# Optimization experiments

Hardware: AMD Instinct MI355X
Metric: run time of the kernel (lower is better)

Reference implementation:

```python
import jax, jax.numpy as jnp
import numpy as np

N_SRC = 50000   # e.g. users
N_DST = 50000   # e.g. items
N = N_SRC + N_DST
E = 1_600_000   # edges (avg degree ~16)
D = 64          # in_size == out_size


def _xavier(key, shape):
    # xavier_uniform for Linear(weight shape [out, in])
    fan_out, fan_in = shape
    limit = jnp.sqrt(6.0 / (fan_in + fan_out)).astype(jnp.float32)
    return jax.random.uniform(key, shape, jnp.float32, -limit, limit)


def setup_inputs() -> dict:
    key = jax.random.key(0)
    ks = jax.random.split(key, 8)
    return {
        "src_embedding": jax.random.normal(ks[0], (N_SRC, D), jnp.float32),
        "dst_embedding": jax.random.normal(ks[1], (N_DST, D), jnp.float32),
        "norm": jax.random.uniform(ks[2], (E, 1), jnp.float32),
        "W1": _xavier(ks[3], (D, D)),
        "b1": jnp.zeros((D,), jnp.float32),
        "W2": _xavier(ks[4], (D, D)),
        "b2": jnp.zeros((D,), jnp.float32),
        "edges_src": jax.random.randint(ks[5], (E,), 0, N, dtype=jnp.int32),
        "edges_dst": jax.random.randint(ks[6], (E,), 0, N, dtype=jnp.int32),
    }


def reference(src_embedding, dst_embedding, norm, W1, b1, W2, b2,
              edges_src, edges_dst):
    # concat user/item node tables: [N, D]
    x = jnp.concatenate([src_embedding, dst_embedding], axis=0)
    xs = x[edges_src]                      # [E, D] gather (edge source nodes)
    xd = x[edges_dst]                      # [E, D] gather (edge dest nodes)
    # msgs = W1(x_src) + W2(x_src * x_dst), per edge
    msgs = (jnp.einsum('ed,od->eo', xs, W1) + b1
            + jnp.einsum('ed,od->eo', xs * xd, W2) + b2)   # [E, D]
    msgs = norm * msgs                     # per-edge scalar normalization
    # copy_e + sum: scatter-sum messages onto destination nodes
    h = jax.ops.segment_sum(msgs, edges_dst, num_segments=N)  # [N, D]
    # LeakyReLU(0.2); dropout is identity in eval / p=0
    return jnp.where(h > 0, h, 0.2 * h)
```

## Files before the change

### kernel.cpp

```cpp
#include <hip/hip_runtime.h>
#include <hip/hip_bf16.h>


#define CHUNK 4096
#define NBMAX 1024
#define BCAP  2304

typedef __attribute__((ext_vector_type(8))) short short8v;
typedef __attribute__((ext_vector_type(4))) float f32x4;
union U4S8 { uint4 u; short8v s; };

__device__ __forceinline__ unsigned int f2bf(float f) {
    unsigned int u = __float_as_uint(f);
    u += 0x7fffu + ((u >> 16) & 1u);
    return u >> 16;
}
__device__ __forceinline__ unsigned int pkbf(float lo, float hi) {
    return (f2bf(hi) << 16) | f2bf(lo);
}

__global__ __launch_bounds__(256) void prep_init_kernel(
    const float* __restrict__ srcEmb, const float* __restrict__ dstEmb,
    unsigned int* __restrict__ xbf, int* __restrict__ gcur,
    int Ntot, int n_src, int NB)
{
    int i = blockIdx.x * 256 + threadIdx.x;
    if (i < NB) gcur[i] = i * BCAP;
    if (i >= Ntot * 32) return;
    int n = i >> 5, w = i & 31;
    const float* row = (n < n_src) ? srcEmb + (size_t)n * 64
                                   : dstEmb + (size_t)(n - n_src) * 64;
    xbf[i] = (f2bf(row[w + 32]) << 16) | f2bf(row[w]);
}

__global__ __launch_bounds__(1024) void part_scatter_kernel(
    const int* __restrict__ es, const int* __restrict__ ed,
    const float* __restrict__ norm, int* __restrict__ gcur,
    uint2* __restrict__ epk, int E, int NB)
{
    __shared__ int   bcnt[NBMAX];
    __shared__ int   lstart[NBMAX];
    __shared__ int   gbase[NBMAX];
    __shared__ int   sc[NBMAX];
    __shared__ uint2 sorted[CHUNK];

    int t  = threadIdx.x;
    int e0 = blockIdx.x * CHUNK;

    bcnt[t] = 0;
    __syncthreads();

    int dreg[4];
    #pragma unroll
    for (int k = 0; k < 4; ++k) {
        int e = e0 + t + k * 1024;
        dreg[k] = (e < E) ? ed[e] : -1;
        if (dreg[k] >= 0) atomicAdd(&bcnt[dreg[k] >> 7], 1);
    }
    __syncthreads();

    int c = (t < NB) ? bcnt[t] : 0;
    sc[t] = c;
    __syncthreads();
    for (int off = 1; off < NBMAX; off <<= 1) {
        int x = 0;
        if (t >= off) x = sc[t - off];
        __syncthreads();
        if (t >= off) sc[t] += x;
        __syncthreads();
    }
    int ex = sc[t] - c;
    lstart[t] = ex;
    bcnt[t]   = ex;
    if (c > 0) gbase[t] = atomicAdd(&gcur[t], c);
    __syncthreads();

    #pragma unroll
    for (int k = 0; k < 4; ++k) {
        int e = e0 + t + k * 1024;
        if (dreg[k] >= 0) {
            unsigned int q = (unsigned int)(norm[e] * 32767.f + 0.5f);
            if (q > 32767u) q = 32767u;
            int lp = atomicAdd(&bcnt[dreg[k] >> 7], 1);
            uint2 r; r.x = (unsigned int)es[e];
            r.y = ((unsigned int)dreg[k] << 15) | q;
            sorted[lp] = r;
        }
    }
    __syncthreads();

    int total = E - e0; if (total > CHUNK) total = CHUNK;
    for (int i = t; i < total; i += 1024) {
        uint2 r = sorted[i];
        int b = (int)(r.y >> 22);
        int gpos = gbase[b] + (i - lstart[b]);
        if (gpos < (b + 1) * BCAP)
            epk[gpos] = r;
    }
}

__global__ __launch_bounds__(512) void bucket_sort_kernel(
    const int* __restrict__ gcur, const uint2* __restrict__ epk,
    uint2* __restrict__ epk2, int* __restrict__ offsets2)
{
    __shared__ int bh[128];
    __shared__ int sc[128];

    int b = blockIdx.x, t = threadIdx.x;
    int base  = b * BCAP;
    int total = gcur[b] - base;
    if (total > BCAP) total = BCAP;

    if (t < 128) bh[t] = 0;
    __syncthreads();
    for (int i = t; i < total; i += 512)
        atomicAdd(&bh[(epk[base + i].y >> 15) & 127], 1);
    __syncthreads();

    int v = 0;
    if (t < 128) { v = bh[t]; sc[t] = v; }
    __syncthreads();
    for (int off = 1; off < 128; off <<= 1) {
        int x = 0;
        if (t < 128 && t >= off) x = sc[t - off];
        __syncthreads();
        if (t < 128 && t >= off) sc[t] += x;
        __syncthreads();
    }
    if (t < 128) {
        int ex = sc[t] - v;
        offsets2[b * 129 + t] = ex;
        if (t == 127) offsets2[b * 129 + 128] = sc[127];
        bh[t] = ex;
    }
    __syncthreads();

    for (int i = t; i < total; i += 512) {
        uint2 r = epk[base + i];
        int pos = atomicAdd(&bh[(r.y >> 15) & 127], 1);
        epk2[base + pos] = r;
    }
}

__global__ __launch_bounds__(256) void accumulate_kernel(
    const unsigned int* __restrict__ xbf,
    const int* __restrict__ offsets2, const uint2* __restrict__ epk2,
    unsigned int* __restrict__ Acat, float* __restrict__ cnt, int Ntot)
{
    int idx  = blockIdx.x * 256 + threadIdx.x;
    int n    = idx >> 6;
    int lane = idx & 63;
    if (n >= Ntot) return;
    int sl  = lane & 7;
    int g   = lane >> 3;
    int b   = n >> 7;
    int loc = n & 127;

    int s0 = b * BCAP + offsets2[b * 129 + loc];
    int s1 = b * BCAP + offsets2[b * 129 + loc + 1];

    float ax0 = 0.f, ax1 = 0.f, ax2 = 0.f, ax3 = 0.f;
    float ay0 = 0.f, ay1 = 0.f, ay2 = 0.f, ay3 = 0.f;
    float c = 0.f;

    for (int base = s0; base < s1; base += 64) {
        int m = s1 - base; if (m > 64) m = 64;
        unsigned int px = 0u, py = 0u;
        if (lane < m) { uint2 pk = epk2[base + lane]; px = pk.x; py = pk.y; }
        for (int k = 0; k < m; k += 16) {
            unsigned int sx0 = __shfl(px, k + g);
            unsigned int sy0 = __shfl(py, k + g);
            unsigned int sx1 = __shfl(px, k + 8 + g);
            unsigned int sy1 = __shfl(py, k + 8 + g);
            uint4 u0 = *(const uint4*)(xbf + (size_t)sx0 * 32 + 4 * sl);
            uint4 u1 = *(const uint4*)(xbf + (size_t)sx1 * 32 + 4 * sl);
            float w0 = (float)(sy0 & 0x7fffu) * (1.f / 32767.f);
            float w1 = (float)(sy1 & 0x7fffu) * (1.f / 32767.f);
            ax0 = fmaf(w0, __uint_as_float(u0.x << 16), ax0);
            ax1 = fmaf(w0, __uint_as_float(u0.y << 16), ax1);
            ax2 = fmaf(w0, __uint_as_float(u0.z << 16), ax2);
            ax3 = fmaf(w0, __uint_as_float(u0.w << 16), ax3);
            ay0 = fmaf(w0, __uint_as_float(u0.x & 0xffff0000u), ay0);
            ay1 = fmaf(w0, __uint_as_float(u0.y & 0xffff0000u), ay1);
            ay2 = fmaf(w0, __uint_as_float(u0.z & 0xffff0000u), ay2);
            ay3 = fmaf(w0, __uint_as_float(u0.w & 0xffff0000u), ay3);
            c += w0;
            ax0 = fmaf(w1, __uint_as_float(u1.x << 16), ax0);
            ax1 = fmaf(w1, __uint_as_float(u1.y << 16), ax1);
            ax2 = fmaf(w1, __uint_as_float(u1.z << 16), ax2);
            ax3 = fmaf(w1, __uint_as_float(u1.w << 16), ax3);
            ay0 = fmaf(w1, __uint_as_float(u1.x & 0xffff0000u), ay0);
            ay1 = fmaf(w1, __uint_as_float(u1.y & 0xffff0000u), ay1);
            ay2 = fmaf(w1, __uint_as_float(u1.z & 0xffff0000u), ay2);
            ay3 = fmaf(w1, __uint_as_float(u1.w & 0xffff0000u), ay3);
            c += w1;
        }
    }

    #pragma unroll
    for (int off = 8; off < 64; off <<= 1) {
        ax0 += __shfl_xor(ax0, off); ax1 += __shfl_xor(ax1, off);
        ax2 += __shfl_xor(ax2, off); ax3 += __shfl_xor(ax3, off);
        ay0 += __shfl_xor(ay0, off); ay1 += __shfl_xor(ay1, off);
        ay2 += __shfl_xor(ay2, off); ay3 += __shfl_xor(ay3, off);
        c   += __shfl_xor(c,   off);
    }

    if (g == 0) {
        uint4 xv = *(const uint4*)(xbf + (size_t)n * 32 + 4 * sl);
        float xl0 = __uint_as_float(xv.x << 16);
        float xl1 = __uint_as_float(xv.y << 16);
        float xl2 = __uint_as_float(xv.z << 16);
        float xl3 = __uint_as_float(xv.w << 16);
        float xh0 = __uint_as_float(xv.x & 0xffff0000u);
        float xh1 = __uint_as_float(xv.y & 0xffff0000u);
        float xh2 = __uint_as_float(xv.z & 0xffff0000u);
        float xh3 = __uint_as_float(xv.w & 0xffff0000u);

        uint4 w0;
        w0.x = pkbf(ax0, ax1);
        w0.y = pkbf(ax2, ax3);
        w0.z = pkbf(ay0, ay1);
        w0.w = pkbf(ay2, ay3);
        uint4 w1;
        w1.x = pkbf(ax0 * xl0, ax1 * xl1);
        w1.y = pkbf(ax2 * xl2, ax3 * xl3);
        w1.z = pkbf(ay0 * xh0, ay1 * xh1);
        w1.w = pkbf(ay2 * xh2, ay3 * xh3);
        *(uint4*)(Acat + (size_t)n * 64 + 4 * sl)      = w0;
        *(uint4*)(Acat + (size_t)n * 64 + 32 + 4 * sl) = w1;
        if (sl == 0) cnt[n] = c;
    }
}

__global__ __launch_bounds__(256) void node_gemm_kernel(
    const unsigned int* __restrict__ Acat, const float* __restrict__ cnt,
    const float* __restrict__ W1, const float* __restrict__ b1,
    const float* __restrict__ W2, const float* __restrict__ b2,
    float* __restrict__ out, int Ntot)
{
    __shared__ unsigned int wlds[64 * 68];

    int t     = threadIdx.x;
    int lane  = t & 63;
    int wv    = t >> 6;
    int base  = blockIdx.x * 64;
    int row16 = lane & 15;
    int q     = lane >> 4;

    int arow = base + wv * 16 + row16;
    if (arow >= Ntot) arow = Ntot - 1;
    const uint4* ap = (const uint4*)(Acat + (size_t)arow * 64);
    uint4 af[4];
    #pragma unroll
    for (int s = 0; s < 4; ++s) af[s] = ap[s * 4 + q];

    for (int i = t; i < 64 * 64; i += 256) {
        int o = i >> 6, j = i & 63;
        int jj = j & 31, sl = jj >> 2, tt = jj & 3;
        int d0 = 4 * sl + ((tt & 1) << 1) + ((tt & 2) ? 32 : 0);
        const float* wsrc = (j < 32) ? W1 : W2;
        wlds[o * 68 + j] = pkbf(wsrc[o * 64 + d0], wsrc[o * 64 + d0 + 1]);
    }

    float cload[4];
    #pragma unroll
    for (int r = 0; r < 4; ++r) {
        int grow = base + wv * 16 + q * 4 + r;
        cload[r] = cnt[grow < Ntot ? grow : (Ntot - 1)];
    }
    f32x4 acc[4];
    #pragma unroll
    for (int j = 0; j < 4; ++j) {
        int col = j * 16 + row16;
        float bs = b1[col] + b2[col];
        #pragma unroll
        for (int r = 0; r < 4; ++r) acc[j][r] = cload[r] * bs;
    }
    __syncthreads();

    #pragma unroll
    for (int s = 0; s < 4; ++s) {
        U4S8 a; a.u = af[s];
        #pragma unroll
        for (int j = 0; j < 4; ++j) {
            int o = j * 16 + row16;
            U4S8 bb; bb.u = *(const uint4*)(wlds + o * 68 + s * 16 + q * 4);
            acc[j] = __builtin_amdgcn_mfma_f32_16x16x32_bf16(
                a.s, bb.s, acc[j], 0, 0, 0);
        }
    }

    #pragma unroll
    for (int r = 0; r < 4; ++r) {
        int grow = base + wv * 16 + q * 4 + r;
        if (grow < Ntot) {
            #pragma unroll
            for (int j = 0; j < 4; ++j) {
                float a = acc[j][r];
                out[(size_t)grow * 64 + j * 16 + row16] = (a > 0.f) ? a : 0.2f * a;
            }
        }
    }
}

extern "C" void kernel_launch(void* const* d_in, const int* in_sizes, int n_in,
                              void* d_out, int out_size, void* d_ws, size_t ws_size,
                              hipStream_t stream) {
    const float* srcEmb = (const float*)d_in[0];
    const float* dstEmb = (const float*)d_in[1];
    const float* norm   = (const float*)d_in[2];
    const float* W1     = (const float*)d_in[3];
    const float* b1     = (const float*)d_in[4];
    const float* W2     = (const float*)d_in[5];
    const float* b2     = (const float*)d_in[6];
    const int*   es     = (const int*)d_in[7];
    const int*   ed     = (const int*)d_in[8];

    const int n_src = in_sizes[0] / 64;
    const int n_dst = in_sizes[1] / 64;
    const int Ntot  = n_src + n_dst;
    const int E     = in_sizes[7];
    const int NB    = (Ntot + 127) >> 7;

    float* cnt      = (float*)d_ws;
    int*   gcur     = (int*)(cnt + Ntot);
    int*   offsets2 = gcur + NB;
    size_t off4     = (size_t)Ntot + NB + (size_t)NB * 129;
    off4 = (off4 + 3) & ~(size_t)3;
    uint2* epk      = (uint2*)((float*)d_ws + off4);
    uint2* epk2     = epk + (size_t)NB * BCAP;
    unsigned int* xbf = (unsigned int*)(epk2 + (size_t)NB * BCAP);
    unsigned int* Acat = (unsigned int*)d_out;

    prep_init_kernel<<<(Ntot * 32 + 255) / 256, 256, 0, stream>>>(
        srcEmb, dstEmb, xbf, gcur, Ntot, n_src, NB);

    part_scatter_kernel<<<(E + CHUNK - 1) / CHUNK, 1024, 0, stream>>>(
        es, ed, norm, gcur, epk, E, NB);

    bucket_sort_kernel<<<NB, 512, 0, stream>>>(gcur, epk, epk2, offsets2);

    accumulate_kernel<<<(Ntot + 3) / 4, 256, 0, stream>>>(
        xbf, offsets2, epk2, Acat, cnt, Ntot);

    node_gemm_kernel<<<(Ntot + 63) / 64, 256, 0, stream>>>(
        Acat, cnt, W1, b1, W2, b2, (float*)d_out, Ntot);
}
```

Baseline: 198.5 us.

## Map one node per 8 lanes in accumulate kernel instead of per wavefront

The accumulate kernel now assigns each destination node to 8 threads instead of a full 64-lane wavefront. Each 8-lane group walks that node's edges sequentially, two at a time, so the cross-group shuffle reduction and the idle lanes in low-degree nodes go away. Launch size shrinks to match. The cost is that lanes in a wavefront now handle different nodes with different degrees, which adds divergence. Each edge record is also loaded redundantly by the 8 lanes of a group.

Result: slower. 206.9 us (+4.2%).

```diff
diff --git a/kernel.cpp b/kernel.cpp
--- a/kernel.cpp
+++ b/kernel.cpp
@@ -147,12 +147,10 @@
     const int* __restrict__ offsets2, const uint2* __restrict__ epk2,
     unsigned int* __restrict__ Acat, float* __restrict__ cnt, int Ntot)
 {
-    int idx  = blockIdx.x * 256 + threadIdx.x;
-    int n    = idx >> 6;
-    int lane = idx & 63;
+    int idx = blockIdx.x * 256 + threadIdx.x;
+    int n   = idx >> 3;
     if (n >= Ntot) return;
-    int sl  = lane & 7;
-    int g   = lane >> 3;
+    int sl  = threadIdx.x & 7;
     int b   = n >> 7;
     int loc = n & 127;
 
@@ -163,74 +161,56 @@
     float ay0 = 0.f, ay1 = 0.f, ay2 = 0.f, ay3 = 0.f;
     float c = 0.f;
 
-    for (int base = s0; base < s1; base += 64) {
-        int m = s1 - base; if (m > 64) m = 64;
-        unsigned int px = 0u, py = 0u;
-        if (lane < m) { uint2 pk = epk2[base + lane]; px = pk.x; py = pk.y; }
-        for (int k = 0; k < m; k += 16) {
-            unsigned int sx0 = __shfl(px, k + g);
-            unsigned int sy0 = __shfl(py, k + g);
-            unsigned int sx1 = __shfl(px, k + 8 + g);
-            unsigned int sy1 = __shfl(py, k + 8 + g);
-            uint4 u0 = *(const uint4*)(xbf + (size_t)sx0 * 32 + 4 * sl);
-            uint4 u1 = *(const uint4*)(xbf + (size_t)sx1 * 32 + 4 * sl);
-            float w0 = (float)(sy0 & 0x7fffu) * (1.f / 32767.f);
-            float w1 = (float)(sy1 & 0x7fffu) * (1.f / 32767.f);
-            ax0 = fmaf(w0, __uint_as_float(u0.x << 16), ax0);
-            ax1 = fmaf(w0, __uint_as_float(u0.y << 16), ax1);
-            ax2 = fmaf(w0, __uint_as_float(u0.z << 16), ax2);
-            ax3 = fmaf(w0, __uint_as_float(u0.w << 16), ax3);
-            ay0 = fmaf(w0, __uint_as_float(u0.x & 0xffff0000u), ay0);
-            ay1 = fmaf(w0, __uint_as_float(u0.y & 0xffff0000u), ay1);
-            ay2 = fmaf(w0, __uint_as_float(u0.z & 0xffff0000u), ay2);
-            ay3 = fmaf(w0, __uint_as_float(u0.w & 0xffff0000u), ay3);
-            c += w0;
-            ax0 = fmaf(w1, __uint_as_float(u1.x << 16), ax0);
-            ax1 = fmaf(w1, __uint_as_float(u1.y << 16), ax1);
-            ax2 = fmaf(w1, __uint_as_float(u1.z << 16), ax2);
-            ax3 = fmaf(w1, __uint_as_float(u1.w << 16), ax3);
-            ay0 = fmaf(w1, __uint_as_float(u1.x & 0xffff0000u), ay0);
-            ay1 = fmaf(w1, __uint_as_float(u1.y & 0xffff0000u), ay1);
-            ay2 = fmaf(w1, __uint_as_float(u1.z & 0xffff0000u), ay2);
-            ay3 = fmaf(w1, __uint_as_float(u1.w & 0xffff0000u), ay3);
-            c += w1;
-        }
-    }
-
-    #pragma unroll
-    for (int off = 8; off < 64; off <<= 1) {
-        ax0 += __shfl_xor(ax0, off); ax1 += __shfl_xor(ax1, off);
-        ax2 += __shfl_xor(ax2, off); ax3 += __shfl_xor(ax3, off);
-        ay0 += __shfl_xor(ay0, off); ay1 += __shfl_xor(ay1, off);
-        ay2 += __shfl_xor(ay2, off); ay3 += __shfl_xor(ay3, off);
-        c   += __shfl_xor(c,   off);
-    }
-
-    if (g == 0) {
-        uint4 xv = *(const uint4*)(xbf + (size_t)n * 32 + 4 * sl);
-        float xl0 = __uint_as_float(xv.x << 16);
-        float xl1 = __uint_as_float(xv.y << 16);
-        float xl2 = __uint_as_float(xv.z << 16);
-        float xl3 = __uint_as_float(xv.w << 16);
-        float xh0 = __uint_as_float(xv.x & 0xffff0000u);
-        float xh1 = __uint_as_float(xv.y & 0xffff0000u);
-        float xh2 = __uint_as_float(xv.z & 0xffff0000u);
-        float xh3 = __uint_as_float(xv.w & 0xffff0000u);
-
-        uint4 w0;
-        w0.x = pkbf(ax0, ax1);
-        w0.y = pkbf(ax2, ax3);
-        w0.z = pkbf(ay0, ay1);
-        w0.w = pkbf(ay2, ay3);
-        uint4 w1;
-        w1.x = pkbf(ax0 * xl0, ax1 * xl1);
-        w1.y = pkbf(ax2 * xl2, ax3 * xl3);
-        w1.z = pkbf(ay0 * xh0, ay1 * xh1);
-        w1.w = pkbf(ay2 * xh2, ay3 * xh3);
-        *(uint4*)(Acat + (size_t)n * 64 + 4 * sl)      = w0;
-        *(uint4*)(Acat + (size_t)n * 64 + 32 + 4 * sl) = w1;
-        if (sl == 0) cnt[n] = c;
-    }
+    for (int r = s0; r < s1; r += 2) {
+        uint2 p0 = epk2[r];
+        int ok1  = (r + 1 < s1);
+        uint2 p1 = epk2[ok1 ? r + 1 : r];
+        uint4 u0 = *(const uint4*)(xbf + (size_t)p0.x * 32 + 4 * sl);
+        uint4 u1 = *(const uint4*)(xbf + (size_t)p1.x * 32 + 4 * sl);
+        float w0 = (float)(p0.y & 0x7fffu) * (1.f / 32767.f);
+        float w1 = ok1 ? (float)(p1.y & 0x7fffu) * (1.f / 32767.f) : 0.f;
+        ax0 = fmaf(w0, __uint_as_float(u0.x << 16), ax0);
+        ax1 = fmaf(w0, __uint_as_float(u0.y << 16), ax1);
+        ax2 = fmaf(w0, __uint_as_float(u0.z << 16), ax2);
+        ax3 = fmaf(w0, __uint_as_float(u0.w << 16), ax3);
+        ay0 = fmaf(w0, __uint_as_float(u0.x & 0xffff0000u), ay0);
+        ay1 = fmaf(w0, __uint_as_float(u0.y & 0xffff0000u), ay1);
+        ay2 = fmaf(w0, __uint_as_float(u0.z & 0xffff0000u), ay2);
+        ay3 = fmaf(w0, __uint_as_float(u0.w & 0xffff0000u), ay3);
+        ax0 = fmaf(w1, __uint_as_float(u1.x << 16), ax0);
+        ax1 = fmaf(w1, __uint_as_float(u1.y << 16), ax1);
+        ax2 = fmaf(w1, __uint_as_float(u1.z << 16), ax2);
+        ax3 = fmaf(w1, __uint_as_float(u1.w << 16), ax3);
+        ay0 = fmaf(w1, __uint_as_float(u1.x & 0xffff0000u), ay0);
+        ay1 = fmaf(w1, __uint_as_float(u1.y & 0xffff0000u), ay1);
+        ay2 = fmaf(w1, __uint_as_float(u1.z & 0xffff0000u), ay2);
+        ay3 = fmaf(w1, __uint_as_float(u1.w & 0xffff0000u), ay3);
+        c += w0 + w1;
+    }
+
+    uint4 xv = *(const uint4*)(xbf + (size_t)n * 32 + 4 * sl);
+    float xl0 = __uint_as_float(xv.x << 16);
+    float xl1 = __uint_as_float(xv.y << 16);
+    float xl2 = __uint_as_float(xv.z << 16);
+    float xl3 = __uint_as_float(xv.w << 16);
+    float xh0 = __uint_as_float(xv.x & 0xffff0000u);
+    float xh1 = __uint_as_float(xv.y & 0xffff0000u);
+    float xh2 = __uint_as_float(xv.z & 0xffff0000u);
+    float xh3 = __uint_as_float(xv.w & 0xffff0000u);
+
+    uint4 w0;
+    w0.x = pkbf(ax0, ax1);
+    w0.y = pkbf(ax2, ax3);
+    w0.z = pkbf(ay0, ay1);
+    w0.w = pkbf(ay2, ay3);
+    uint4 w1;
+    w1.x = pkbf(ax0 * xl0, ax1 * xl1);
+    w1.y = pkbf(ax2 * xl2, ax3 * xl3);
+    w1.z = pkbf(ay0 * xh0, ay1 * xh1);
+    w1.w = pkbf(ay2 * xh2, ay3 * xh3);
+    *(uint4*)(Acat + (size_t)n * 64 + 4 * sl)      = w0;
+    *(uint4*)(Acat + (size_t)n * 64 + 32 + 4 * sl) = w1;
+    if (sl == 0) cnt[n] = c;
 }
 
 __global__ __launch_bounds__(256) void node_gemm_kernel(
@@ -341,7 +321,7 @@
 
     bucket_sort_kernel<<<NB, 512, 0, stream>>>(gcur, epk, epk2, offsets2);
 
-    accumulate_kernel<<<(Ntot + 3) / 4, 256, 0, stream>>>(
+    accumulate_kernel<<<(Ntot * 8 + 255) / 256, 256, 0, stream>>>(
         xbf, offsets2, epk2, Acat, cnt, Ntot);
 
     node_gemm_kernel<<<(Ntot + 63) / 64, 256, 0, stream>>>(
```

## Fuse bucket sort and accumulation into one kernel using shared-memory sorted edges

Applied to the files above, without the earlier changes.

Merges the per-bucket counting sort with the per-node gather-accumulate, so each 512-thread block sorts its bucket's edges into LDS and then its 8 waves accumulate the 128 nodes of that bucket. This removes the global epk2/offsets2 round trip and one kernel launch. In exchange, parallelism drops to one block per 128 nodes (about 782 blocks), each using roughly 19KB of LDS. Waves also process nodes serially, which may reduce latency hiding for the random xbf gathers.

After: 199.4 us. About the same (+0.4%).

```diff
diff --git a/kernel.cpp b/kernel.cpp
--- a/kernel.cpp
+++ b/kernel.cpp
@@ -99,12 +99,15 @@
     }
 }
 
-__global__ __launch_bounds__(512) void bucket_sort_kernel(
+__global__ __launch_bounds__(512) void accum_fused_kernel(
+    const unsigned int* __restrict__ xbf,
     const int* __restrict__ gcur, const uint2* __restrict__ epk,
-    uint2* __restrict__ epk2, int* __restrict__ offsets2)
+    unsigned int* __restrict__ Acat, float* __restrict__ cnt, int Ntot)
 {
-    __shared__ int bh[128];
-    __shared__ int sc[128];
+    __shared__ uint2 srt[BCAP];
+    __shared__ int   bh[128];
+    __shared__ int   sc[128];
+    __shared__ int   offs[129];
 
     int b = blockIdx.x, t = threadIdx.x;
     int base  = b * BCAP;
@@ -129,8 +132,8 @@
     }
     if (t < 128) {
         int ex = sc[t] - v;
-        offsets2[b * 129 + t] = ex;
-        if (t == 127) offsets2[b * 129 + 128] = sc[127];
+        offs[t] = ex;
+        if (t == 127) offs[128] = sc[127];
         bh[t] = ex;
     }
     __syncthreads();
@@ -138,98 +141,93 @@
     for (int i = t; i < total; i += 512) {
         uint2 r = epk[base + i];
         int pos = atomicAdd(&bh[(r.y >> 15) & 127], 1);
-        epk2[base + pos] = r;
-    }
-}
-
-__global__ __launch_bounds__(256) void accumulate_kernel(
-    const unsigned int* __restrict__ xbf,
-    const int* __restrict__ offsets2, const uint2* __restrict__ epk2,
-    unsigned int* __restrict__ Acat, float* __restrict__ cnt, int Ntot)
-{
-    int idx  = blockIdx.x * 256 + threadIdx.x;
-    int n    = idx >> 6;
-    int lane = idx & 63;
-    if (n >= Ntot) return;
-    int sl  = lane & 7;
-    int g   = lane >> 3;
-    int b   = n >> 7;
-    int loc = n & 127;
-
-    int s0 = b * BCAP + offsets2[b * 129 + loc];
-    int s1 = b * BCAP + offsets2[b * 129 + loc + 1];
-
-    float ax0 = 0.f, ax1 = 0.f, ax2 = 0.f, ax3 = 0.f;
-    float ay0 = 0.f, ay1 = 0.f, ay2 = 0.f, ay3 = 0.f;
-    float c = 0.f;
-
-    for (int base = s0; base < s1; base += 64) {
-        int m = s1 - base; if (m > 64) m = 64;
-        unsigned int px = 0u, py = 0u;
-        if (lane < m) { uint2 pk = epk2[base + lane]; px = pk.x; py = pk.y; }
-        for (int k = 0; k < m; k += 16) {
-            unsigned int sx0 = __shfl(px, k + g);
-            unsigned int sy0 = __shfl(py, k + g);
-            unsigned int sx1 = __shfl(px, k + 8 + g);
-            unsigned int sy1 = __shfl(py, k + 8 + g);
-            uint4 u0 = *(const uint4*)(xbf + (size_t)sx0 * 32 + 4 * sl);
-            uint4 u1 = *(const uint4*)(xbf + (size_t)sx1 * 32 + 4 * sl);
-            float w0 = (float)(sy0 & 0x7fffu) * (1.f / 32767.f);
-            float w1 = (float)(sy1 & 0x7fffu) * (1.f / 32767.f);
-            ax0 = fmaf(w0, __uint_as_float(u0.x << 16), ax0);
-            ax1 = fmaf(w0, __uint_as_float(u0.y << 16), ax1);
-            ax2 = fmaf(w0, __uint_as_float(u0.z << 16), ax2);
-            ax3 = fmaf(w0, __uint_as_float(u0.w << 16), ax3);
-            ay0 = fmaf(w0, __uint_as_float(u0.x & 0xffff0000u), ay0);
-            ay1 = fmaf(w0, __uint_as_float(u0.y & 0xffff0000u), ay1);
-            ay2 = fmaf(w0, __uint_as_float(u0.z & 0xffff0000u), ay2);
-            ay3 = fmaf(w0, __uint_as_float(u0.w & 0xffff0000u), ay3);
-            c += w0;
-            ax0 = fmaf(w1, __uint_as_float(u1.x << 16), ax0);
-            ax1 = fmaf(w1, __uint_as_float(u1.y << 16), ax1);
-            ax2 = fmaf(w1, __uint_as_float(u1.z << 16), ax2);
-            ax3 = fmaf(w1, __uint_as_float(u1.w << 16), ax3);
-            ay0 = fmaf(w1, __uint_as_float(u1.x & 0xffff0000u), ay0);
-            ay1 = fmaf(w1, __uint_as_float(u1.y & 0xffff0000u), ay1);
-            ay2 = fmaf(w1, __uint_as_float(u1.z & 0xffff0000u), ay2);
-            ay3 = fmaf(w1, __uint_as_float(u1.w & 0xffff0000u), ay3);
-            c += w1;
-        }
-    }
-
-    #pragma unroll
-    for (int off = 8; off < 64; off <<= 1) {
-        ax0 += __shfl_xor(ax0, off); ax1 += __shfl_xor(ax1, off);
-        ax2 += __shfl_xor(ax2, off); ax3 += __shfl_xor(ax3, off);
-        ay0 += __shfl_xor(ay0, off); ay1 += __shfl_xor(ay1, off);
-        ay2 += __shfl_xor(ay2, off); ay3 += __shfl_xor(ay3, off);
-        c   += __shfl_xor(c,   off);
-    }
-
-    if (g == 0) {
-        uint4 xv = *(const uint4*)(xbf + (size_t)n * 32 + 4 * sl);
-        float xl0 = __uint_as_float(xv.x << 16);
-        float xl1 = __uint_as_float(xv.y << 16);
-        float xl2 = __uint_as_float(xv.z << 16);
-        float xl3 = __uint_as_float(xv.w << 16);
-        float xh0 = __uint_as_float(xv.x & 0xffff0000u);
-        float xh1 = __uint_as_float(xv.y & 0xffff0000u);
-        float xh2 = __uint_as_float(xv.z & 0xffff0000u);
-        float xh3 = __uint_as_float(xv.w & 0xffff0000u);
-
-        uint4 w0;
-        w0.x = pkbf(ax0, ax1);
-        w0.y = pkbf(ax2, ax3);
-        w0.z = pkbf(ay0, ay1);
-        w0.w = pkbf(ay2, ay3);
-        uint4 w1;
-        w1.x = pkbf(ax0 * xl0, ax1 * xl1);
-        w1.y = pkbf(ax2 * xl2, ax3 * xl3);
-        w1.z = pkbf(ay0 * xh0, ay1 * xh1);
-        w1.w = pkbf(ay2 * xh2, ay3 * xh3);
-        *(uint4*)(Acat + (size_t)n * 64 + 4 * sl)      = w0;
-        *(uint4*)(Acat + (size_t)n * 64 + 32 + 4 * sl) = w1;
-        if (sl == 0) cnt[n] = c;
+        srt[pos] = r;
+    }
+    __syncthreads();
+
+    int lane = t & 63;
+    int wv   = t >> 6;
+    int sl   = lane & 7;
+    int g    = lane >> 3;
+
+    for (int li = 0; li < 16; ++li) {
+        int loc = wv + li * 8;
+        int n   = b * 128 + loc;
+        int s0  = offs[loc];
+        int s1  = offs[loc + 1];
+
+        float ax0 = 0.f, ax1 = 0.f, ax2 = 0.f, ax3 = 0.f;
+        float ay0 = 0.f, ay1 = 0.f, ay2 = 0.f, ay3 = 0.f;
+        float c = 0.f;
+
+        for (int bs2 = s0; bs2 < s1; bs2 += 64) {
+            int m = s1 - bs2; if (m > 64) m = 64;
+            unsigned int px = 0u, py = 0u;
+            if (lane < m) { uint2 pk = srt[bs2 + lane]; px = pk.x; py = pk.y; }
+            for (int k = 0; k < m; k += 16) {
+                unsigned int sx0 = __shfl(px, k + g);
+                unsigned int sy0 = __shfl(py, k + g);
+                unsigned int sx1 = __shfl(px, k + 8 + g);
+                unsigned int sy1 = __shfl(py, k + 8 + g);
+                uint4 u0 = *(const uint4*)(xbf + (size_t)sx0 * 32 + 4 * sl);
+                uint4 u1 = *(const uint4*)(xbf + (size_t)sx1 * 32 + 4 * sl);
+                float w0 = (float)(sy0 & 0x7fffu) * (1.f / 32767.f);
+                float w1 = (float)(sy1 & 0x7fffu) * (1.f / 32767.f);
+                ax0 = fmaf(w0, __uint_as_float(u0.x << 16), ax0);
+                ax1 = fmaf(w0, __uint_as_float(u0.y << 16), ax1);
+                ax2 = fmaf(w0, __uint_as_float(u0.z << 16), ax2);
+                ax3 = fmaf(w0, __uint_as_float(u0.w << 16), ax3);
+                ay0 = fmaf(w0, __uint_as_float(u0.x & 0xffff0000u), ay0);
+                ay1 = fmaf(w0, __uint_as_float(u0.y & 0xffff0000u), ay1);
+                ay2 = fmaf(w0, __uint_as_float(u0.z & 0xffff0000u), ay2);
+                ay3 = fmaf(w0, __uint_as_float(u0.w & 0xffff0000u), ay3);
+                c += w0;
+                ax0 = fmaf(w1, __uint_as_float(u1.x << 16), ax0);
+                ax1 = fmaf(w1, __uint_as_float(u1.y << 16), ax1);
+                ax2 = fmaf(w1, __uint_as_float(u1.z << 16), ax2);
+                ax3 = fmaf(w1, __uint_as_float(u1.w << 16), ax3);
+                ay0 = fmaf(w1, __uint_as_float(u1.x & 0xffff0000u), ay0);
+                ay1 = fmaf(w1, __uint_as_float(u1.y & 0xffff0000u), ay1);
+                ay2 = fmaf(w1, __uint_as_float(u1.z & 0xffff0000u), ay2);
+                ay3 = fmaf(w1, __uint_as_float(u1.w & 0xffff0000u), ay3);
+                c += w1;
+            }
+        }
+
+        #pragma unroll
+        for (int off = 8; off < 64; off <<= 1) {
+            ax0 += __shfl_xor(ax0, off); ax1 += __shfl_xor(ax1, off);
+            ax2 += __shfl_xor(ax2, off); ax3 += __shfl_xor(ax3, off);
+            ay0 += __shfl_xor(ay0, off); ay1 += __shfl_xor(ay1, off);
+            ay2 += __shfl_xor(ay2, off); ay3 += __shfl_xor(ay3, off);
+            c   += __shfl_xor(c,   off);
+        }
+
+        if (g == 0 && n < Ntot) {
+            uint4 xv = *(const uint4*)(xbf + (size_t)n * 32 + 4 * sl);
+            float xl0 = __uint_as_float(xv.x << 16);
+            float xl1 = __uint_as_float(xv.y << 16);
+            float xl2 = __uint_as_float(xv.z << 16);
+            float xl3 = __uint_as_float(xv.w << 16);
+            float xh0 = __uint_as_float(xv.x & 0xffff0000u);
+            float xh1 = __uint_as_float(xv.y & 0xffff0000u);
+            float xh2 = __uint_as_float(xv.z & 0xffff0000u);
+            float xh3 = __uint_as_float(xv.w & 0xffff0000u);
+
+            uint4 w0;
+            w0.x = pkbf(ax0, ax1);
+            w0.y = pkbf(ax2, ax3);
+            w0.z = pkbf(ay0, ay1);
+            w0.w = pkbf(ay2, ay3);
+            uint4 w1;
+            w1.x = pkbf(ax0 * xl0, ax1 * xl1);
+            w1.y = pkbf(ax2 * xl2, ax3 * xl3);
+            w1.z = pkbf(ay0 * xh0, ay1 * xh1);
+            w1.w = pkbf(ay2 * xh2, ay3 * xh3);
+            *(uint4*)(Acat + (size_t)n * 64 + 4 * sl)      = w0;
+            *(uint4*)(Acat + (size_t)n * 64 + 32 + 4 * sl) = w1;
+            if (sl == 0) cnt[n] = c;
+        }
     }
 }
 
@@ -325,12 +323,10 @@
 
     float* cnt      = (float*)d_ws;
     int*   gcur     = (int*)(cnt + Ntot);
-    int*   offsets2 = gcur + NB;
-    size_t off4     = (size_t)Ntot + NB + (size_t)NB * 129;
+    size_t off4     = (size_t)Ntot + NB;
     off4 = (off4 + 3) & ~(size_t)3;
     uint2* epk      = (uint2*)((float*)d_ws + off4);
-    uint2* epk2     = epk + (size_t)NB * BCAP;
-    unsigned int* xbf = (unsigned int*)(epk2 + (size_t)NB * BCAP);
+    unsigned int* xbf = (unsigned int*)(epk + (size_t)NB * BCAP);
     unsigned int* Acat = (unsigned int*)d_out;
 
     prep_init_kernel<<<(Ntot * 32 + 255) / 256, 256, 0, stream>>>(
@@ -339,10 +335,8 @@
     part_scatter_kernel<<<(E + CHUNK - 1) / CHUNK, 1024, 0, stream>>>(
         es, ed, norm, gcur, epk, E, NB);
 
-    bucket_sort_kernel<<<NB, 512, 0, stream>>>(gcur, epk, epk2, offsets2);
-
-    accumulate_kernel<<<(Ntot + 3) / 4, 256, 0, stream>>>(
-        xbf, offsets2, epk2, Acat, cnt, Ntot);
+    accum_fused_kernel<<<NB, 512, 0, stream>>>(
+        xbf, gcur, epk, Acat, cnt, Ntot);
 
     node_gemm_kernel<<<(Ntot + 63) / 64, 256, 0, stream>>>(
         Acat, cnt, W1, b1, W2, b2, (float*)d_out, Ntot);
```
